# Optimization experiments

Measured on AMD Instinct MI355X. Metric: run time of the kernel, lower is better.

The kernel has to match this reference:

```python
import jax, jax.numpy as jnp
import numpy as np

NUM_CLASSES = 21
BBOX_NUM = 2
BG_CLASS = 20          # nums_classes - 1
NMS_THR = 0.5
CLASS_OFFSET = 4096.0  # batched-NMS trick: shift boxes per class so IoU across classes is 0


def setup_inputs() -> dict:
    key = jax.random.key(0)
    # post-backbone feature map: C = bbox_num*5 + num_classes = 31, 28x28 grid (stride-32 on 896 image)
    features = jax.random.normal(key, (64, 31, 28, 28), dtype=jnp.float32)
    return {"features": features, "h_ori": 896, "w_ori": 896}


def _pairwise_iou(b):
    # b: [N, 4] (x1, y1, x2, y2) -> [N, N] IoU
    x1 = jnp.maximum(b[:, None, 0], b[None, :, 0])
    y1 = jnp.maximum(b[:, None, 1], b[None, :, 1])
    x2 = jnp.minimum(b[:, None, 2], b[None, :, 2])
    y2 = jnp.minimum(b[:, None, 3], b[None, :, 3])
    inter = jnp.clip(x2 - x1, 0.0) * jnp.clip(y2 - y1, 0.0)
    area = jnp.clip(b[:, 2] - b[:, 0], 0.0) * jnp.clip(b[:, 3] - b[:, 1], 0.0)
    union = area[:, None] + area[None, :] - inter
    return inter / jnp.maximum(union, 1e-9)


def _nms(boxes, scores, cats, valid):
    # class-aware greedy NMS on a single image; returns bool keep mask [N]
    N = boxes.shape[0]
    obox = boxes + (cats.astype(boxes.dtype) * CLASS_OFFSET)[:, None]
    s = jnp.where(valid, scores, -jnp.inf)
    order = jnp.argsort(-s)                 # descending score
    iou = _pairwise_iou(obox[order])        # [N, N] among sorted boxes
    idx = jnp.arange(N)

    def body(i, keep):
        ki = keep[i]
        suppress = (iou[i] > NMS_THR) & (idx > i) & ki
        return keep & ~suppress

    keep_sorted = jax.lax.fori_loop(0, N, body, valid[order])
    return jnp.zeros(N, bool).at[order].set(keep_sorted)


def reference(features, h_ori, w_ori):
    B, C, Hf, Wf = features.shape
    N = Hf * Wf
    # permute_and_flatten: [B, C, H, W] -> [B, H*W, C]
    x = features.transpose(0, 2, 3, 1).reshape(B, N, C)

    con_idx = jnp.arange(4, BBOX_NUM * 5, 5)            # confidence channels
    pred_conf = x[:, :, con_idx]                        # [B, N, bbox_num]
    pred_bbox = jax.nn.sigmoid(x[:, :, :BBOX_NUM * 5])  # [B, N, bbox_num*5]
    pred_class = jax.nn.softmax(x[:, :, BBOX_NUM * 5:], axis=-1)  # [B, N, num_classes]

    conf_max = jnp.max(pred_conf, axis=-1)              # [B, N]
    conf_arg = jnp.argmax(pred_conf, axis=-1)           # [B, N]
    con_prob = conf_max[..., None] * pred_class
    prob = jnp.max(con_prob, axis=-1)                   # [B, N]
    cat = jnp.argmax(con_prob, axis=-1)                 # [B, N]

    # Boxer.filter_bboxes: gather the 4 coords of the max-confidence box (offset = argmax*5)
    gidx = (conf_arg * 5)[..., None] + jnp.arange(4)    # [B, N, 4]
    box = jnp.take_along_axis(pred_bbox, gidx, axis=-1) # (x, y, w, h) in grid units

    # grid_cell_2_bbox (inverse of config_gt encoding), cell idx = row*Wf + col
    col = (jnp.arange(N) % Wf).astype(box.dtype)
    row = (jnp.arange(N) // Wf).astype(box.dtype)
    cx = (box[..., 0] + col) * (w_ori / Wf)
    cy = (box[..., 1] + row) * (h_ori / Hf)
    bw = box[..., 2] * w_ori
    bh = box[..., 3] * h_ori
    # convert center xywh -> corners
    boxes = jnp.stack([cx - bw / 2, cy - bh / 2, cx + bw / 2, cy + bh / 2], axis=-1)

    valid = cat != BG_CLASS                             # background filtering
    keep = jax.vmap(_nms)(boxes, prob, cat, valid)      # per-image NMS

    # fixed-shape packed output: [x1, y1, x2, y2, prob, cat, keep] -> [B, N, 7]
    out = jnp.concatenate(
        [boxes, prob[..., None], cat.astype(jnp.float32)[..., None],
         jnp.where(keep, 1.0, 0.0)[..., None]], axis=-1)
    return out
```

## Files before the change

kernel.cpp:

```cpp
#include <hip/hip_runtime.h>

#define BATCH 64
#define CH 31
#define HF 28
#define WF 28
#define NCELL 784
#define NCLS 21
#define BGCLS 20
#define CAP 128
#define NMS_THR 0.5f

__device__ __forceinline__ float bcast_f(float v, int l) {
    return __int_as_float(__builtin_amdgcn_readlane(__float_as_int(v), l));
}
__device__ __forceinline__ unsigned long long shfl_xor_u64(unsigned long long v, int j) {
    int lo = __shfl_xor((int)(unsigned)(v & 0xFFFFFFFFull), j, 64);
    int hi = __shfl_xor((int)(unsigned)(v >> 32), j, 64);
    return ((unsigned long long)(unsigned)hi << 32) | (unsigned)lo;
}

#define CEX0(VAR, J, UP) { unsigned long long p_ = shfl_xor_u64(VAR, (J));     \
    bool tm_ = (((lane & (J)) == 0) == (UP));                                  \
    VAR = ((VAR < p_) == tm_) ? VAR : p_; }

__global__ __launch_bounds__(256)
void decode_kernel(const float* __restrict__ feat,
                   const int* __restrict__ hofp,
                   const int* __restrict__ wofp,
                   float* __restrict__ out,
                   float4* __restrict__ wbox,
                   unsigned long long* __restrict__ wkey)
{
    int gid = blockIdx.x * blockDim.x + threadIdx.x;
    if (gid >= BATCH * NCELL) return;
    int b = gid / NCELL;
    int n = gid - b * NCELL;

    const float* base = feat + (size_t)b * CH * NCELL + n;
    float x[CH];
#pragma unroll
    for (int c = 0; c < CH; ++c) x[c] = base[(size_t)c * NCELL];

    float c0 = x[4], c1 = x[9];
    int carg = (c1 > c0) ? 1 : 0;
    float cmax = fmaxf(c0, c1);

    float m = x[10];
#pragma unroll
    for (int k = 1; k < NCLS; ++k) m = fmaxf(m, x[10 + k]);
    float e[NCLS];
    float sum = 0.0f;
#pragma unroll
    for (int k = 0; k < NCLS; ++k) { e[k] = expf(x[10 + k] - m); sum += e[k]; }

    float best = -INFINITY;
    int cat = 0;
#pragma unroll
    for (int k = 0; k < NCLS; ++k) {
        float cp = cmax * (e[k] / sum);
        if (cp > best) { best = cp; cat = k; }
    }

    float rx = carg ? x[5] : x[0];
    float ry = carg ? x[6] : x[1];
    float rw = carg ? x[7] : x[2];
    float rh = carg ? x[8] : x[3];
    rx = 1.0f / (1.0f + expf(-rx));
    ry = 1.0f / (1.0f + expf(-ry));
    rw = 1.0f / (1.0f + expf(-rw));
    rh = 1.0f / (1.0f + expf(-rh));

    float w_ori = (float)(*wofp), h_ori = (float)(*hofp);
    float sw = w_ori / (float)WF, sh = h_ori / (float)HF;
    float col = (float)(n % WF), row = (float)(n / WF);
    float cx = (rx + col) * sw;
    float cy = (ry + row) * sh;
    float bw = rw * w_ori;
    float bh = rh * h_ori;
    float x1 = cx - bw * 0.5f, y1 = cy - bh * 0.5f;
    float x2 = cx + bw * 0.5f, y2 = cy + bh * 0.5f;

    float* o = out + (size_t)gid * 7;
    o[0] = x1; o[1] = y1; o[2] = x2; o[3] = y2;
    o[4] = best; o[5] = (float)cat; o[6] = 0.0f;

    float off = (float)cat * 4096.0f;
    wbox[gid] = make_float4(x1 + off, y1 + off, x2 + off, y2 + off);

    unsigned long long key = ~0ull;
    if (cat != BGCLS) {
        unsigned u = __float_as_uint(best);
        u = (u & 0x80000000u) ? ~u : (u | 0x80000000u);
        key = ((unsigned long long)(~u) << 15) |
              ((unsigned long long)cat << 10) | (unsigned)n;
    }
    wkey[gid] = key;
}

__global__ __launch_bounds__(64)
void nms_kernel(const float4* __restrict__ wbox,
                const unsigned long long* __restrict__ wkey,
                float* __restrict__ out)
{
    const int blk = blockIdx.x;
    const int b = blk / (NCLS - 1);
    const int c = blk - b * (NCLS - 1);
    const int lane = threadIdx.x;

    __shared__ unsigned long long lbuf[CAP];
    lbuf[lane] = ~0ull;
    lbuf[64 + lane] = ~0ull;

    int base = 0;
    const unsigned long long* wk = wkey + (size_t)b * NCELL;
#pragma unroll
    for (int it = 0; it < 13; ++it) {
        int cell = it * 64 + lane;
        bool m2 = false;
        unsigned long long key = ~0ull;
        if (cell < NCELL) {
            key = wk[cell];
            m2 = (((key >> 10) & 31ull) == (unsigned long long)c);
        }
        unsigned long long bal = __ballot(m2);
        if (m2) {
            int pos = base + __popcll(bal & ((1ull << lane) - 1ull));
            if (pos < CAP) lbuf[pos] = key;
        }
        base += (int)__popcll(bal);
    }
    __syncthreads();
    int n = base > CAP ? CAP : base;
    if (n == 0) return;

    unsigned long long k0 = lbuf[lane];
    unsigned long long k1 = lbuf[64 + lane];
    bool two = (n > 64);

    if (!two) {
#pragma unroll
        for (int k = 2; k <= 64; k <<= 1) {
            bool up = ((lane & k) == 0);
#pragma unroll
            for (int j = k >> 1; j >= 1; j >>= 1) CEX0(k0, j, up)
        }
    } else {
#pragma unroll
        for (int k = 2; k <= 32; k <<= 1) {
            bool up = ((lane & k) == 0);
#pragma unroll
            for (int j = k >> 1; j >= 1; j >>= 1) { CEX0(k0, j, up) CEX0(k1, j, up) }
        }
#pragma unroll
        for (int j = 32; j >= 1; j >>= 1) { CEX0(k0, j, true) CEX0(k1, j, false) }
        {
            unsigned long long mn = (k0 < k1) ? k0 : k1;
            unsigned long long mx = (k0 < k1) ? k1 : k0;
            k0 = mn; k1 = mx;
        }
#pragma unroll
        for (int j = 32; j >= 1; j >>= 1) { CEX0(k0, j, true) CEX0(k1, j, true) }
    }

    int cell0 = (int)(k0 & 1023ull);
    int cell1 = (int)(k1 & 1023ull);
    bool ok0 = (lane < n);
    bool ok1 = (64 + lane) < n;

    const float4* wb = wbox + (size_t)b * NCELL;
    float4 B0 = wb[ok0 ? cell0 : 0];
    float a0 = fmaxf(B0.z - B0.x, 0.f) * fmaxf(B0.w - B0.y, 0.f);
    float4 B1 = make_float4(0.f, 0.f, 0.f, 0.f);
    float a1 = 0.f;
    if (two) {
        B1 = wb[ok1 ? cell1 : 0];
        a1 = fmaxf(B1.z - B1.x, 0.f) * fmaxf(B1.w - B1.y, 0.f);
    }

    unsigned long long keep0 = (n >= 64) ? ~0ull : ((1ull << n) - 1);
    unsigned long long keep1 = two ? ((n >= 128) ? ~0ull : ((1ull << (n - 64)) - 1))
                                   : 0ull;

    unsigned long long rem = keep0;
    while (rem) {
        int i = __builtin_ctzll(rem);
        rem &= rem - 1;
        float ix1 = bcast_f(B0.x, i), iy1 = bcast_f(B0.y, i);
        float ix2 = bcast_f(B0.z, i), iy2 = bcast_f(B0.w, i);
        float ia  = bcast_f(a0, i);
        {
            float xx1 = fmaxf(ix1, B0.x), yy1 = fmaxf(iy1, B0.y);
            float xx2 = fminf(ix2, B0.z), yy2 = fminf(iy2, B0.w);
            float inter = fmaxf(xx2 - xx1, 0.f) * fmaxf(yy2 - yy1, 0.f);
            float uni = ia + a0 - inter;
            bool s = (inter / fmaxf(uni, 1e-9f)) > NMS_THR;
            unsigned long long mm = __ballot(s) & keep0;
            mm &= (i < 63) ? (~0ull << (i + 1)) : 0ull;
            keep0 &= ~mm; rem &= ~mm;
        }
        if (two) {
            float xx1 = fmaxf(ix1, B1.x), yy1 = fmaxf(iy1, B1.y);
            float xx2 = fminf(ix2, B1.z), yy2 = fminf(iy2, B1.w);
            float inter = fmaxf(xx2 - xx1, 0.f) * fmaxf(yy2 - yy1, 0.f);
            float uni = ia + a1 - inter;
            bool s = (inter / fmaxf(uni, 1e-9f)) > NMS_THR;
            keep1 &= ~(__ballot(s) & keep1);
        }
    }
    if (two) {
        unsigned long long rem1 = keep1;
        while (rem1) {
            int i = __builtin_ctzll(rem1);
            rem1 &= rem1 - 1;
            float ix1 = bcast_f(B1.x, i), iy1 = bcast_f(B1.y, i);
            float ix2 = bcast_f(B1.z, i), iy2 = bcast_f(B1.w, i);
            float ia  = bcast_f(a1, i);
            float xx1 = fmaxf(ix1, B1.x), yy1 = fmaxf(iy1, B1.y);
            float xx2 = fminf(ix2, B1.z), yy2 = fminf(iy2, B1.w);
            float inter = fmaxf(xx2 - xx1, 0.f) * fmaxf(yy2 - yy1, 0.f);
            float uni = ia + a1 - inter;
            bool s = (inter / fmaxf(uni, 1e-9f)) > NMS_THR;
            unsigned long long mm = __ballot(s) & keep1;
            mm &= (i < 63) ? (~0ull << (i + 1)) : 0ull;
            keep1 &= ~mm; rem1 &= ~mm;
        }
    }

    if (ok0 && ((keep0 >> lane) & 1ull))
        out[((size_t)b * NCELL + cell0) * 7 + 6] = 1.0f;
    if (two && ok1 && ((keep1 >> lane) & 1ull))
        out[((size_t)b * NCELL + cell1) * 7 + 6] = 1.0f;
}

extern "C" void kernel_launch(void* const* d_in, const int* in_sizes, int n_in,
                              void* d_out, int out_size, void* d_ws, size_t ws_size,
                              hipStream_t stream) {
    const float* feat = (const float*)d_in[0];
    const int* h_ori  = (const int*)d_in[1];
    const int* w_ori  = (const int*)d_in[2];
    float* out = (float*)d_out;

    float4* wbox = (float4*)d_ws;
    unsigned long long* wkey =
        (unsigned long long*)((char*)d_ws + sizeof(float4) * BATCH * NCELL);

    int total = BATCH * NCELL;
    decode_kernel<<<(total + 255) / 256, 256, 0, stream>>>(
        feat, h_ori, w_ori, out, wbox, wkey);
    nms_kernel<<<BATCH * (NCLS - 1), 64, 0, stream>>>(wbox, wkey, out);
}
```

Before: 26.07 us.

## Bucket candidates per class with atomics in decode and rank-sort in NMS

The decode kernel now appends each non-background candidate key to a per-(image,class) list using an atomic counter, instead of writing a dense key array that every NMS block rescans. The NMS block reads only its own list and sorts it by computing each element's rank through a shared-memory all-pairs comparison, replacing the bitonic shuffle network. It also swaps the softmax divide for a reciprocal multiply. The cost is an extra memset launch and atomic contention. The shared-memory reads and writes are ordered only by s_waitcnt, with no barrier, which is safe only because the block is a single wavefront.

Result: slower. 30.84 us (+18.3%).

```diff
diff --git a/kernel.cpp b/kernel.cpp
--- a/kernel.cpp
+++ b/kernel.cpp
@@ -13,15 +13,6 @@
 __device__ __forceinline__ float bcast_f(float v, int l) {
     return __int_as_float(__builtin_amdgcn_readlane(__float_as_int(v), l));
 }
-__device__ __forceinline__ unsigned long long shfl_xor_u64(unsigned long long v, int j) {
-    int lo = __shfl_xor((int)(unsigned)(v & 0xFFFFFFFFull), j, 64);
-    int hi = __shfl_xor((int)(unsigned)(v >> 32), j, 64);
-    return ((unsigned long long)(unsigned)hi << 32) | (unsigned)lo;
-}
-
-#define CEX0(VAR, J, UP) { unsigned long long p_ = shfl_xor_u64(VAR, (J));     \
-    bool tm_ = (((lane & (J)) == 0) == (UP));                                  \
-    VAR = ((VAR < p_) == tm_) ? VAR : p_; }
 
 __global__ __launch_bounds__(256)
 void decode_kernel(const float* __restrict__ feat,
@@ -29,7 +20,8 @@
                    const int* __restrict__ wofp,
                    float* __restrict__ out,
                    float4* __restrict__ wbox,
-                   unsigned long long* __restrict__ wkey)
+                   unsigned long long* __restrict__ lists,
+                   int* __restrict__ cnt)
 {
     int gid = blockIdx.x * blockDim.x + threadIdx.x;
     if (gid >= BATCH * NCELL) return;
@@ -52,12 +44,13 @@
     float sum = 0.0f;
 #pragma unroll
     for (int k = 0; k < NCLS; ++k) { e[k] = expf(x[10 + k] - m); sum += e[k]; }
+    float rinv = 1.0f / sum;
 
     float best = -INFINITY;
     int cat = 0;
 #pragma unroll
     for (int k = 0; k < NCLS; ++k) {
-        float cp = cmax * (e[k] / sum);
+        float cp = cmax * (e[k] * rinv);
         if (cp > best) { best = cp; cat = k; }
     }
 
@@ -87,85 +80,60 @@
     float off = (float)cat * 4096.0f;
     wbox[gid] = make_float4(x1 + off, y1 + off, x2 + off, y2 + off);
 
-    unsigned long long key = ~0ull;
     if (cat != BGCLS) {
         unsigned u = __float_as_uint(best);
         u = (u & 0x80000000u) ? ~u : (u | 0x80000000u);
-        key = ((unsigned long long)(~u) << 15) |
-              ((unsigned long long)cat << 10) | (unsigned)n;
-    }
-    wkey[gid] = key;
+        unsigned long long key =
+            ((unsigned long long)(~u) << 10) | (unsigned)n;
+        int bc = b * (NCLS - 1) + cat;
+        int slot = atomicAdd(&cnt[bc], 1);
+        if (slot < CAP) lists[(size_t)bc * CAP + slot] = key;
+    }
 }
 
 __global__ __launch_bounds__(64)
 void nms_kernel(const float4* __restrict__ wbox,
-                const unsigned long long* __restrict__ wkey,
+                const unsigned long long* __restrict__ lists,
+                const int* __restrict__ cnt,
                 float* __restrict__ out)
 {
     const int blk = blockIdx.x;
     const int b = blk / (NCLS - 1);
-    const int c = blk - b * (NCLS - 1);
     const int lane = threadIdx.x;
 
-    __shared__ unsigned long long lbuf[CAP];
-    lbuf[lane] = ~0ull;
-    lbuf[64 + lane] = ~0ull;
-
-    int base = 0;
-    const unsigned long long* wk = wkey + (size_t)b * NCELL;
-#pragma unroll
-    for (int it = 0; it < 13; ++it) {
-        int cell = it * 64 + lane;
-        bool m2 = false;
-        unsigned long long key = ~0ull;
-        if (cell < NCELL) {
-            key = wk[cell];
-            m2 = (((key >> 10) & 31ull) == (unsigned long long)c);
-        }
-        unsigned long long bal = __ballot(m2);
-        if (m2) {
-            int pos = base + __popcll(bal & ((1ull << lane) - 1ull));
-            if (pos < CAP) lbuf[pos] = key;
-        }
-        base += (int)__popcll(bal);
-    }
-    __syncthreads();
-    int n = base > CAP ? CAP : base;
+    int n = cnt[blk];
+    if (n > CAP) n = CAP;
     if (n == 0) return;
 
-    unsigned long long k0 = lbuf[lane];
-    unsigned long long k1 = lbuf[64 + lane];
+    const unsigned long long* gl = lists + (size_t)blk * CAP;
+    unsigned long long m0 = (lane < n) ? gl[lane] : ~0ull;
     bool two = (n > 64);
-
-    if (!two) {
-#pragma unroll
-        for (int k = 2; k <= 64; k <<= 1) {
-            bool up = ((lane & k) == 0);
-#pragma unroll
-            for (int j = k >> 1; j >= 1; j >>= 1) CEX0(k0, j, up)
-        }
-    } else {
-#pragma unroll
-        for (int k = 2; k <= 32; k <<= 1) {
-            bool up = ((lane & k) == 0);
-#pragma unroll
-            for (int j = k >> 1; j >= 1; j >>= 1) { CEX0(k0, j, up) CEX0(k1, j, up) }
-        }
-#pragma unroll
-        for (int j = 32; j >= 1; j >>= 1) { CEX0(k0, j, true) CEX0(k1, j, false) }
-        {
-            unsigned long long mn = (k0 < k1) ? k0 : k1;
-            unsigned long long mx = (k0 < k1) ? k1 : k0;
-            k0 = mn; k1 = mx;
-        }
-#pragma unroll
-        for (int j = 32; j >= 1; j >>= 1) { CEX0(k0, j, true) CEX0(k1, j, true) }
-    }
+    unsigned long long m1 = (two && 64 + lane < n) ? gl[64 + lane] : ~0ull;
+
+    __shared__ unsigned long long lb[CAP];
+    __shared__ unsigned long long lb2[CAP];
+    lb[lane] = m0;
+    lb[64 + lane] = m1;
+    asm volatile("s_waitcnt lgkmcnt(0)" ::: "memory");
+
+    int r0 = 0, r1 = 0;
+    for (int j = 0; j < n; ++j) {
+        unsigned long long kj = lb[j];
+        r0 += (kj < m0) ? 1 : 0;
+        r1 += (kj < m1) ? 1 : 0;
+    }
+    if (lane < n) lb2[r0] = m0;
+    if (two && 64 + lane < n) lb2[r1] = m1;
+    asm volatile("s_waitcnt lgkmcnt(0)" ::: "memory");
+
+    bool ok0 = (lane < n);
+    bool ok1 = two && ((64 + lane) < n);
+    unsigned long long k0 = ok0 ? lb2[lane] : ~0ull;
+    unsigned long long k1 = ok1 ? lb2[64 + lane] : ~0ull;
+    asm volatile("s_waitcnt lgkmcnt(0)" ::: "memory");
 
     int cell0 = (int)(k0 & 1023ull);
     int cell1 = (int)(k1 & 1023ull);
-    bool ok0 = (lane < n);
-    bool ok1 = (64 + lane) < n;
 
     const float4* wb = wbox + (size_t)b * NCELL;
     float4 B0 = wb[ok0 ? cell0 : 0];
@@ -228,7 +196,7 @@
 
     if (ok0 && ((keep0 >> lane) & 1ull))
         out[((size_t)b * NCELL + cell0) * 7 + 6] = 1.0f;
-    if (two && ok1 && ((keep1 >> lane) & 1ull))
+    if (ok1 && ((keep1 >> lane) & 1ull))
         out[((size_t)b * NCELL + cell1) * 7 + 6] = 1.0f;
 }
 
@@ -241,11 +209,15 @@
     float* out = (float*)d_out;
 
     float4* wbox = (float4*)d_ws;
-    unsigned long long* wkey =
-        (unsigned long long*)((char*)d_ws + sizeof(float4) * BATCH * NCELL);
+    char* p = (char*)d_ws + sizeof(float4) * BATCH * NCELL;
+    int* cnt = (int*)p;
+    unsigned long long* lists =
+        (unsigned long long*)(p + sizeof(int) * BATCH * (NCLS - 1));
+
+    hipMemsetAsync(cnt, 0, sizeof(int) * BATCH * (NCLS - 1), stream);
 
     int total = BATCH * NCELL;
     decode_kernel<<<(total + 255) / 256, 256, 0, stream>>>(
-        feat, h_ori, w_ori, out, wbox, wkey);
-    nms_kernel<<<BATCH * (NCLS - 1), 64, 0, stream>>>(wbox, wkey, out);
-}
+        feat, h_ori, w_ori, out, wbox, lists, cnt);
+    nms_kernel<<<BATCH * (NCLS - 1), 64, 0, stream>>>(wbox, lists, cnt, out);
+}
```
